# Kernel tuning notes

Measured on AMD Instinct MI355X. Metric: run time of the kernel, lower is better.

Reference implementation:

```python
import jax, jax.numpy as jnp
import numpy as np

EPS = 1e-6      # zero-token detection eps
LN_EPS = 1e-5   # torch LayerNorm default
H = 8           # num_heads


def setup_inputs() -> dict:
    key = jax.random.key(0)
    ks = jax.random.split(key, 6)
    B, T, D = 4, 2048, 512
    embs = jax.random.normal(ks[0], (B, T, D), jnp.float32)
    labels = jax.random.uniform(ks[1], (B, T), jnp.float32)
    s = 1.0 / np.sqrt(D)
    ln_g = jnp.ones((D,), jnp.float32)
    ln_b = jnp.zeros((D,), jnp.float32)
    in_proj_w = jax.random.uniform(ks[2], (3 * D, D), jnp.float32, -s, s)
    in_proj_b = jnp.zeros((3 * D,), jnp.float32)
    out_w = jax.random.uniform(ks[3], (D, D), jnp.float32, -s, s)
    out_b = jnp.zeros((D,), jnp.float32)
    alpha = jnp.float32(1.0)
    beta = jnp.float32(0.0)
    return {"embs": embs, "labels": labels, "ln_g": ln_g, "ln_b": ln_b,
            "in_proj_w": in_proj_w, "in_proj_b": in_proj_b,
            "out_w": out_w, "out_b": out_b, "alpha": alpha, "beta": beta}


def reference(embs, labels, ln_g, ln_b, in_proj_w, in_proj_b, out_w, out_b, alpha, beta):
    B, T, D = embs.shape
    h, dh = H, D // H
    # pre-LayerNorm
    mu = embs.mean(-1, keepdims=True)
    var = ((embs - mu) ** 2).mean(-1, keepdims=True)
    x = (embs - mu) / jnp.sqrt(var + LN_EPS) * ln_g + ln_b
    # key padding mask from all-zero tokens (computed on normalized x, as in source)
    kpm = jnp.abs(x).sum(-1) <= EPS                      # [B,T] bool
    w = jnp.where(kpm, jnp.float32(0.0), labels)         # zero labels on masked tokens
    # fused qkv projection (nn.MultiheadAttention in_proj)
    qkv = x @ in_proj_w.T + in_proj_b                    # [B,T,3D]
    q, k, v = jnp.split(qkv, 3, axis=-1)
    def sp(a):
        return a.reshape(B, T, h, dh).transpose(0, 2, 1, 3)  # [B,h,T,dh]
    q, k, v = sp(q), sp(k), sp(v)
    scores = jnp.einsum('bhqd,bhkd->bhqk', q, k) / np.sqrt(dh)
    # additive label bias: alpha * labels (broadcast over heads & queries) + beta
    scores = scores + (alpha * w[:, None, None, :] + beta)
    # key padding mask -> -inf (use large negative for stability)
    scores = jnp.where(kpm[:, None, None, :], jnp.float32(-1e30), scores)
    a = jax.nn.softmax(scores, axis=-1)
    o = jnp.einsum('bhqk,bhkd->bhqd', a, v).transpose(0, 2, 1, 3).reshape(B, T, D)
    o = o @ out_w.T + out_b
    o = jnp.nan_to_num(o, nan=0.0, posinf=0.0, neginf=0.0)
    # masked mean pool over T
    m = (~kpm)[..., None].astype(o.dtype)                # [B,T,1]
    pooled = (o * m).sum(1) / jnp.maximum(m.sum(1), 1.0)  # [B,D]
    return pooled
```

## Files before the change

kernel.cpp:

```cpp
#include <hip/hip_runtime.h>
#include <math.h>

#define T 2048
#define D 512
#define NH 8
#define DH 64
#define NB 4
#define NTOK (NB * T)
#define LOG2E 1.44269504f
#define QSCALE (0.125f * LOG2E)

using bf16x8 = __attribute__((ext_vector_type(8))) short;
using f32x4  = __attribute__((ext_vector_type(4))) float;

static __device__ __forceinline__ unsigned short f2bf(float f) {
    union { float f; unsigned u; } v; v.f = f;
    unsigned r = v.u + 0x7fffu + ((v.u >> 16) & 1u);
    return (unsigned short)(r >> 16);
}
#if __has_builtin(__builtin_amdgcn_cvt_pk_bf16_f32)
static __device__ __forceinline__ unsigned pack_bf16_pair(float a, float b) {
    auto r = __builtin_amdgcn_cvt_pk_bf16_f32(a, b);
    union { decltype(r) v; unsigned u; } c; c.v = r;
    return c.u;
}
#else
static __device__ __forceinline__ unsigned pack_bf16_pair(float a, float b) {
    union { float f; unsigned u; } ua, ub; ua.f = a; ub.f = b;
    unsigned ra = ua.u + 0x7fffu + ((ua.u >> 16) & 1u);
    unsigned rb = ub.u + 0x7fffu + ((ub.u >> 16) & 1u);
    return __builtin_amdgcn_perm(rb, ra, 0x07060302);
}
#endif


__global__ __launch_bounds__(256) void ln_kernel(
    const float* __restrict__ embs, const float* __restrict__ labels,
    const float* __restrict__ g, const float* __restrict__ bb,
    const float* __restrict__ alpha_p, const float* __restrict__ beta_p,
    unsigned short* __restrict__ xfrag, float* __restrict__ wexp,
    float* __restrict__ kpmf)
{
    __shared__ __align__(16) unsigned short Xs[16][520];
    int tid = threadIdx.x, wave = tid >> 6, lane = tid & 63;
    int quad = lane >> 4, lm = lane & 15;
    int t16 = blockIdx.x;

    float4 g0 = *(const float4*)(g + lane * 8), g1 = *(const float4*)(g + lane * 8 + 4);
    float4 c0 = *(const float4*)(bb + lane * 8), c1 = *(const float4*)(bb + lane * 8 + 4);
    float gv[8] = {g0.x, g0.y, g0.z, g0.w, g1.x, g1.y, g1.z, g1.w};
    float cv[8] = {c0.x, c0.y, c0.z, c0.w, c1.x, c1.y, c1.z, c1.w};

    for (int tt = 0; tt < 4; ++tt) {
        int n = t16 * 16 + wave * 4 + tt;
        const float* e = embs + (size_t)n * D + lane * 8;
        float4 a4 = *(const float4*)e, b4 = *(const float4*)(e + 4);
        float v[8] = {a4.x, a4.y, a4.z, a4.w, b4.x, b4.y, b4.z, b4.w};

        float s = 0.f, ss = 0.f;
        #pragma unroll
        for (int j = 0; j < 8; ++j) { s += v[j]; ss += v[j] * v[j]; }
        #pragma unroll
        for (int o = 1; o <= 32; o <<= 1) {
            s += __shfl_xor(s, o, 64);
            ss += __shfl_xor(ss, o, 64);
        }
        float mu = s * (1.0f / D);
        float var = ss * (1.0f / D) - mu * mu;
        float rstd = rsqrtf(var + 1e-5f);

        float x[8], as = 0.f;
        #pragma unroll
        for (int j = 0; j < 8; ++j) {
            x[j] = (v[j] - mu) * rstd * gv[j] + cv[j];
            as += fabsf(x[j]);
        }
        uint4 pk;
        pk.x = pack_bf16_pair(x[0], x[1]);
        pk.y = pack_bf16_pair(x[2], x[3]);
        pk.z = pack_bf16_pair(x[4], x[5]);
        pk.w = pack_bf16_pair(x[6], x[7]);
        *(uint4*)&Xs[wave * 4 + tt][lane * 8] = pk;

        #pragma unroll
        for (int o = 1; o <= 32; o <<= 1) as += __shfl_xor(as, o, 64);
        if (lane == 0) {
            int kpm = (as <= 1e-6f);
            kpmf[n] = kpm ? 1.0f : 0.0f;
            wexp[n] = kpm ? 0.0f : __expf(alpha_p[0] * labels[n] + beta_p[0]);
        }
    }
    __syncthreads();
    #pragma unroll
    for (int i = 0; i < 4; ++i) {
        int kc = wave * 4 + i;
        bf16x8 fr = *(const bf16x8*)&Xs[lm][kc * 32 + quad * 8];
        *(bf16x8*)(xfrag + ((size_t)(t16 * 16 + kc) * 64 + lane) * 8) = fr;
    }
}

__global__ __launch_bounds__(256) void wconv_kernel(
    const float* __restrict__ w, unsigned short* __restrict__ wbfrag)
{
    __shared__ __align__(16) unsigned short Ws[16][520];
    int tid = threadIdx.x, wave = tid >> 6, lane = tid & 63;
    int quad = lane >> 4, lm = lane & 15;
    int j16 = blockIdx.x;

    for (int tt = 0; tt < 4; ++tt) {
        int j = j16 * 16 + wave * 4 + tt;
        const float* wp = w + (size_t)j * D + lane * 8;
        float4 a4 = *(const float4*)wp, b4 = *(const float4*)(wp + 4);
        uint4 pk;
        pk.x = pack_bf16_pair(a4.x, a4.y);
        pk.y = pack_bf16_pair(a4.z, a4.w);
        pk.z = pack_bf16_pair(b4.x, b4.y);
        pk.w = pack_bf16_pair(b4.z, b4.w);
        *(uint4*)&Ws[wave * 4 + tt][lane * 8] = pk;
    }
    __syncthreads();
    #pragma unroll
    for (int i = 0; i < 4; ++i) {
        int kc = wave * 4 + i;
        bf16x8 fr = *(const bf16x8*)&Ws[lm][kc * 32 + quad * 8];
        *(bf16x8*)(wbfrag + ((size_t)(j16 * 16 + kc) * 64 + lane) * 8) = fr;
    }
}

__global__ __launch_bounds__(256) void wfrag_fill(
    const float* __restrict__ wexp, unsigned short* __restrict__ vfrag)
{
    int idx = blockIdx.x * 256 + threadIdx.x;
    int lane = idx & 63, chunk = idx >> 6;
    int kk = chunk & 1, t64 = (chunk >> 1) & 31, bh = chunk >> 6;
    int lm = lane & 15, quad = lane >> 4;
    int b_ = bh >> 3;
    size_t base = (((size_t)chunk * 5 + 4) * 64 + lane) * 8;
    if (lm == 0) {
        int key0 = t64 * 64 + kk * 32 + quad * 8;
        const float* wp = wexp + b_ * T + key0;
        unsigned short vv[8];
        #pragma unroll
        for (int e = 0; e < 8; ++e) vv[e] = f2bf(wp[e]);
        *(uint4*)(vfrag + base) = *(uint4*)vv;
    } else {
        uint4 z = {0u, 0u, 0u, 0u};
        *(uint4*)(vfrag + base) = z;
    }
}

__global__ __launch_bounds__(256) void qkv_mfma(
    const unsigned short* __restrict__ xfrag, const unsigned short* __restrict__ wbfrag,
    const float* __restrict__ bias, const float* __restrict__ wexp,
    unsigned short* __restrict__ qfrag, unsigned short* __restrict__ kfrag,
    unsigned short* __restrict__ vfrag)
{
    __shared__ __align__(16) unsigned short Ls[4][64][72];
    int tid = threadIdx.x;
    int wave = tid >> 6, lane = tid & 63, quad = lane >> 4, lm = lane & 15;
    int wr = wave >> 1, wc = wave & 1;
    int m0 = blockIdx.x * 128 + wr * 64;
    int j0 = blockIdx.y * 128 + wc * 64;
    int mt16 = m0 >> 4, jt16 = j0 >> 4;

    f32x4 acc[4][4];
    #pragma unroll
    for (int a = 0; a < 4; ++a)
        #pragma unroll
        for (int b = 0; b < 4; ++b) acc[a][b] = (f32x4){0.f,0.f,0.f,0.f};

    bf16x8 af0[4], bf0[4], af1[4], bf1[4];
    auto load_ab = [&](int kc, bf16x8 (&af)[4], bf16x8 (&bf)[4]) {
        #pragma unroll
        for (int mf = 0; mf < 4; ++mf)
            af[mf] = *(const bf16x8*)(xfrag + ((size_t)((mt16 + mf) * 16 + kc) * 64 + lane) * 8);
        #pragma unroll
        for (int nt = 0; nt < 4; ++nt)
            bf[nt] = *(const bf16x8*)(wbfrag + ((size_t)((jt16 + nt) * 16 + kc) * 64 + lane) * 8);
    };
    auto do_mfma = [&](bf16x8 (&af)[4], bf16x8 (&bf)[4]) {
        #pragma unroll
        for (int mf = 0; mf < 4; ++mf)
            #pragma unroll
            for (int nt = 0; nt < 4; ++nt)
                acc[mf][nt] = __builtin_amdgcn_mfma_f32_16x16x32_bf16(af[mf], bf[nt], acc[mf][nt], 0, 0, 0);
    };

    load_ab(0, af0, bf0);
    for (int kc = 0; kc < 16; kc += 2) {
        load_ab(kc + 1, af1, bf1);
        do_mfma(af0, bf0);
        load_ab((kc + 2) & 15, af0, bf0);
        do_mfma(af1, bf1);
    }

    int part = j0 >> 9;
    int h = (j0 & 511) >> 6;
    int b_ = m0 >> 11, tloc = m0 & (T - 1);
    int bh = b_ * NH + h;
    float bcol[4];
    #pragma unroll
    for (int nt = 0; nt < 4; ++nt) bcol[nt] = bias[j0 + nt * 16 + lm];

    if (part == 2) {
        float wv[4][4];
        #pragma unroll
        for (int mf = 0; mf < 4; ++mf)
            #pragma unroll
            for (int r = 0; r < 4; ++r)
                wv[mf][r] = wexp[b_ * T + tloc + mf * 16 + quad * 4 + r];
        #pragma unroll
        for (int mf = 0; mf < 4; ++mf)
            #pragma unroll
            for (int nt = 0; nt < 4; ++nt) {
                uint2 pw;
                pw.x = pack_bf16_pair((acc[mf][nt][0] + bcol[nt]) * wv[mf][0],
                                      (acc[mf][nt][1] + bcol[nt]) * wv[mf][1]);
                pw.y = pack_bf16_pair((acc[mf][nt][2] + bcol[nt]) * wv[mf][2],
                                      (acc[mf][nt][3] + bcol[nt]) * wv[mf][3]);
                *(uint2*)&Ls[wave][nt * 16 + lm][mf * 16 + quad * 4] = pw;
            }
        #pragma unroll
        for (int nt = 0; nt < 4; ++nt)
            #pragma unroll
            for (int kk = 0; kk < 2; ++kk) {
                bf16x8 fr = *(const bf16x8*)&Ls[wave][nt * 16 + lm][kk * 32 + quad * 8];
                size_t chunk = ((((size_t)bh * 32 + (tloc >> 6)) * 2 + kk) * 5) + nt;
                *(bf16x8*)(vfrag + chunk * 512 + lane * 8) = fr;
            }
    } else {
        float scale = (part == 0) ? QSCALE : 1.0f;
        #pragma unroll
        for (int mf = 0; mf < 4; ++mf)
            #pragma unroll
            for (int nt = 0; nt < 4; ++nt)
                #pragma unroll
                for (int r = 0; r < 4; ++r)
                    Ls[wave][mf * 16 + quad * 4 + r][nt * 16 + lm] =
                        f2bf((acc[mf][nt][r] + bcol[nt]) * scale);
        if (part == 0) {
            #pragma unroll
            for (int mf = 0; mf < 4; ++mf)
                #pragma unroll
                for (int kk = 0; kk < 2; ++kk) {
                    bf16x8 fr = *(const bf16x8*)&Ls[wave][mf * 16 + lm][kk * 32 + quad * 8];
                    size_t chunk = ((size_t)bh * 128 + (tloc >> 4) + mf) * 2 + kk;
                    *(bf16x8*)(qfrag + chunk * 512 + lane * 8) = fr;
                }
        } else {
            #pragma unroll
            for (int nta = 0; nta < 4; ++nta)
                #pragma unroll
                for (int kk = 0; kk < 2; ++kk) {
                    bf16x8 fr = *(const bf16x8*)&Ls[wave][lm * 4 + nta][kk * 32 + quad * 8];
                    size_t chunk = ((((size_t)bh * 32 + (tloc >> 6)) * 2 + kk) * 4) + nta;
                    *(bf16x8*)(kfrag + chunk * 512 + lane * 8) = fr;
                }
        }
    }
}

__global__ __launch_bounds__(256, 2) void attn_mfma(
    const unsigned short* __restrict__ qfrag, const unsigned short* __restrict__ kfrag,
    const unsigned short* __restrict__ vfrag, const float* __restrict__ kpmf,
    float* __restrict__ S)
{
    __shared__ __align__(16) unsigned short Ps[4][2][64][72];
    __shared__ float Lx[2][2][64];
    int g = blockIdx.x;
    int bh = g & 31, q0 = (g >> 5) * 128;
    int tid = threadIdx.x, wave = tid >> 6, lane = tid & 63;
    int quad = lane >> 4, lm = lane & 15;
    int qh = wave >> 1, ks = wave & 1;
    int qbase = q0 + qh * 64;
    int b_ = bh >> 3, h = bh & 7;

    bf16x8 qf[4][2];
    int t16b = (qbase >> 4);
    #pragma unroll
    for (int mf = 0; mf < 4; ++mf)
        #pragma unroll
        for (int kk = 0; kk < 2; ++kk)
            qf[mf][kk] = *(const bf16x8*)(qfrag +
                (((size_t)(bh * 128 + t16b + mf) * 2 + kk) * 64 + lane) * 8);

    f32x4 accO[4][4], accL[4];
    #pragma unroll
    for (int mf = 0; mf < 4; ++mf) {
        #pragma unroll
        for (int nt = 0; nt < 4; ++nt) accO[mf][nt] = (f32x4){0.f,0.f,0.f,0.f};
        accL[mf] = (f32x4){0.f,0.f,0.f,0.f};
    }

    const unsigned short* kb = kfrag + (size_t)bh * 32 * 8 * 512 + (size_t)lane * 8;
    const unsigned short* vb = vfrag + (size_t)bh * 32 * 10 * 512 + (size_t)lane * 8;
    int t0k = ks * 16;

    bf16x8 kf[4][2];
    auto load_k = [&](int t64) {
        const unsigned short* p = kb + (size_t)t64 * 8 * 512;
        #pragma unroll
        for (int kk = 0; kk < 2; ++kk)
            #pragma unroll
            for (int nt = 0; nt < 4; ++nt)
                kf[nt][kk] = *(const bf16x8*)(p + ((size_t)kk * 4 + nt) * 512);
    };
    auto load_v = [&](int t64, bf16x8 (&vf)[5][2]) {
        const unsigned short* p = vb + (size_t)t64 * 10 * 512;
        #pragma unroll
        for (int kk = 0; kk < 2; ++kk)
            #pragma unroll
            for (int nt = 0; nt < 5; ++nt)
                vf[nt][kk] = *(const bf16x8*)(p + ((size_t)kk * 5 + nt) * 512);
    };
    auto load_p = [&](int buf, bf16x8 (&pf)[4][2]) {
        #pragma unroll
        for (int mf = 0; mf < 4; ++mf)
            #pragma unroll
            for (int kk = 0; kk < 2; ++kk)
                pf[mf][kk] = *(const bf16x8*)&Ps[wave][buf][mf * 16 + lm][kk * 32 + quad * 8];
    };
    auto qk_exp = [&](int buf) {
        #pragma unroll
        for (int mf = 0; mf < 4; ++mf) {
            f32x4 s[4];
            __builtin_amdgcn_s_setprio(1);
            #pragma unroll
            for (int nt = 0; nt < 4; ++nt) {
                f32x4 t0 = (f32x4){0.f,0.f,0.f,0.f};
                t0 = __builtin_amdgcn_mfma_f32_16x16x32_bf16(qf[mf][0], kf[nt][0], t0, 0, 0, 0);
                t0 = __builtin_amdgcn_mfma_f32_16x16x32_bf16(qf[mf][1], kf[nt][1], t0, 0, 0, 0);
                s[nt] = t0;
            }
            __builtin_amdgcn_s_setprio(0);
            int rowb = mf * 16 + quad * 4;
            #pragma unroll
            for (int r = 0; r < 4; ++r) {
                float p0 = __builtin_amdgcn_exp2f(s[0][r]);
                float p1 = __builtin_amdgcn_exp2f(s[1][r]);
                float p2 = __builtin_amdgcn_exp2f(s[2][r]);
                float p3 = __builtin_amdgcn_exp2f(s[3][r]);
                uint2 pw;
                pw.x = pack_bf16_pair(p0, p1);
                pw.y = pack_bf16_pair(p2, p3);
                *(uint2*)&Ps[wave][buf][rowb + r][lm * 4] = pw;
            }
        }
    };
    auto pv = [&](bf16x8 (&pf)[4][2], bf16x8 (&vf)[5][2]) {
        __builtin_amdgcn_s_setprio(1);
        #pragma unroll
        for (int mf = 0; mf < 4; ++mf) {
            #pragma unroll
            for (int nt = 0; nt < 4; ++nt) {
                accO[mf][nt] = __builtin_amdgcn_mfma_f32_16x16x32_bf16(pf[mf][0], vf[nt][0], accO[mf][nt], 0, 0, 0);
                accO[mf][nt] = __builtin_amdgcn_mfma_f32_16x16x32_bf16(pf[mf][1], vf[nt][1], accO[mf][nt], 0, 0, 0);
            }
            accL[mf] = __builtin_amdgcn_mfma_f32_16x16x32_bf16(pf[mf][0], vf[4][0], accL[mf], 0, 0, 0);
            accL[mf] = __builtin_amdgcn_mfma_f32_16x16x32_bf16(pf[mf][1], vf[4][1], accL[mf], 0, 0, 0);
        }
        __builtin_amdgcn_s_setprio(0);
    };

    load_k(t0k);
    qk_exp(0);
    load_k(t0k + 1);
    for (int t = 1; t < 16; ++t) {
        bf16x8 pf[4][2], vf[5][2];
        load_p((t - 1) & 1, pf);
        load_v(t0k + t - 1, vf);
        qk_exp(t & 1);
        load_k(t0k + ((t + 1) & 15));
        pv(pf, vf);
    }
    {
        bf16x8 pf[4][2], vf[5][2];
        load_p(1, pf);
        load_v(t0k + 15, vf);
        pv(pf, vf);
    }

    if (lm == 0) {
        #pragma unroll
        for (int mf = 0; mf < 4; ++mf)
            #pragma unroll
            for (int r = 0; r < 4; ++r)
                Lx[qh][ks][mf * 16 + quad * 4 + r] = accL[mf][r];
    }
    __syncthreads();

    float pooled[4] = {0.f, 0.f, 0.f, 0.f};
    #pragma unroll
    for (int mf = 0; mf < 4; ++mf)
        #pragma unroll
        for (int r = 0; r < 4; ++r) {
            int rloc = mf * 16 + quad * 4 + r;
            float l = Lx[qh][0][rloc] + Lx[qh][1][rloc];
            float w = (1.0f - kpmf[b_ * T + qbase + rloc]) / l;
            #pragma unroll
            for (int nt = 0; nt < 4; ++nt) pooled[nt] += accO[mf][nt][r] * w;
        }
    #pragma unroll
    for (int nt = 0; nt < 4; ++nt) {
        pooled[nt] += __shfl_xor(pooled[nt], 16, 64);
        pooled[nt] += __shfl_xor(pooled[nt], 32, 64);
    }
    if (quad == 0) {
        #pragma unroll
        for (int nt = 0; nt < 4; ++nt)
            atomicAdd(&S[b_ * D + h * DH + nt * 16 + lm], pooled[nt]);
    }
}

__global__ __launch_bounds__(256) void out_kernel(
    const float* __restrict__ S, const float* __restrict__ kpmf,
    const float* __restrict__ Wo, const float* __restrict__ bo,
    float* __restrict__ out)
{
    __shared__ float Sl[512];
    __shared__ float cs[4];
    __shared__ float pr[4][64];
    int b_ = blockIdx.x >> 3;
    int cg = blockIdx.x & 7;
    int tid = threadIdx.x;
    int col = tid & 63, kq = tid >> 6;
    Sl[tid] = S[b_ * D + tid];
    Sl[tid + 256] = S[b_ * D + tid + 256];
    const float* kp = kpmf + b_ * T;
    float c = 0.f;
    for (int t = tid; t < T; t += 256) c += kp[t];
    #pragma unroll
    for (int o = 32; o; o >>= 1) c += __shfl_xor(c, o, 64);
    if ((tid & 63) == 0) cs[tid >> 6] = c;
    __syncthreads();
    float masked = cs[0] + cs[1] + cs[2] + cs[3];
    float cnt = (float)T - masked;
    float inv = 1.0f / fmaxf(cnt, 1.0f);

    int d = cg * 64 + col;
    const float4* wr4 = (const float4*)(Wo + (size_t)d * D + kq * 128);
    float dot = 0.f;
    #pragma unroll 8
    for (int i = 0; i < 32; ++i) {
        float4 w4 = wr4[i];
        int kbase = kq * 128 + i * 4;
        dot += Sl[kbase + 0] * w4.x + Sl[kbase + 1] * w4.y +
               Sl[kbase + 2] * w4.z + Sl[kbase + 3] * w4.w;
    }
    pr[kq][col] = dot;
    __syncthreads();
    if (kq == 0) {
        float tot = pr[0][col] + pr[1][col] + pr[2][col] + pr[3][col];
        out[b_ * D + d] = (tot + bo[d] * cnt) * inv;
    }
}

extern "C" void kernel_launch(void* const* d_in, const int* in_sizes, int n_in,
                              void* d_out, int out_size, void* d_ws, size_t ws_size,
                              hipStream_t stream) {
    const float* embs   = (const float*)d_in[0];
    const float* labels = (const float*)d_in[1];
    const float* ln_g   = (const float*)d_in[2];
    const float* ln_b   = (const float*)d_in[3];
    const float* ipw    = (const float*)d_in[4];
    const float* ipb    = (const float*)d_in[5];
    const float* ow     = (const float*)d_in[6];
    const float* obb    = (const float*)d_in[7];
    const float* alpha  = (const float*)d_in[8];
    const float* beta   = (const float*)d_in[9];
    float* out = (float*)d_out;

    unsigned short* xfrag  = (unsigned short*)d_ws;
    unsigned short* wbfrag = xfrag + (size_t)NTOK * D;
    unsigned short* qfrag  = wbfrag + (size_t)3 * D * D;
    unsigned short* kfrag  = qfrag + (size_t)NTOK * D;
    unsigned short* vfrag  = kfrag + (size_t)NTOK * D;
    float* wexp = (float*)(vfrag + (size_t)32 * 32 * 2 * 5 * 512);
    float* kpmf = wexp + NTOK;
    float* S    = kpmf + NTOK;

    hipMemsetAsync(S, 0, (size_t)NB * D * sizeof(float), stream);
    ln_kernel<<<NTOK / 16, 256, 0, stream>>>(embs, labels, ln_g, ln_b, alpha, beta,
                                             xfrag, wexp, kpmf);
    wconv_kernel<<<(3 * D) / 16, 256, 0, stream>>>(ipw, wbfrag);
    wfrag_fill<<<512, 256, 0, stream>>>(wexp, vfrag);
    dim3 gq(NTOK / 128, (3 * D) / 128);
    qkv_mfma<<<gq, 256, 0, stream>>>(xfrag, wbfrag, ipb, wexp, qfrag, kfrag, vfrag);
    attn_mfma<<<32 * (T / 128), 256, 0, stream>>>(qfrag, kfrag, vfrag, kpmf, S);
    out_kernel<<<NB * 8, 256, 0, stream>>>(S, kpmf, ow, obb, out);
}
```

Measured before the change: 157.2 us.

## Merge LayerNorm, weight conversion and memset into one prep kernel; fold wexp fill into QKV

Combines the LayerNorm, in-projection weight bf16 conversion and the S-accumulator zeroing into one kernel, using block-index ranges to assign each role. The separate wexp fragment fill kernel is removed, and its work moves into the V epilogue of the QKV GEMM. This cuts the pipeline from six launches (including a memset) to three before attention, removing launch and inter-kernel gap overhead. The cost is some extra divergence and global reads in the QKV epilogue.

Result: faster. 150.6 us, median of 2 (-4.2%).

```diff
diff --git a/kernel.cpp b/kernel.cpp
--- a/kernel.cpp
+++ b/kernel.cpp
@@ -34,118 +34,100 @@
 #endif
 
 
-__global__ __launch_bounds__(256) void ln_kernel(
+__global__ __launch_bounds__(256) void prep_kernel(
     const float* __restrict__ embs, const float* __restrict__ labels,
     const float* __restrict__ g, const float* __restrict__ bb,
     const float* __restrict__ alpha_p, const float* __restrict__ beta_p,
+    const float* __restrict__ ipw,
     unsigned short* __restrict__ xfrag, float* __restrict__ wexp,
-    float* __restrict__ kpmf)
+    float* __restrict__ kpmf, unsigned short* __restrict__ wbfrag,
+    float* __restrict__ S)
 {
-    __shared__ __align__(16) unsigned short Xs[16][520];
+    __shared__ __align__(16) unsigned short Sh[16][520];
+    int blk = blockIdx.x;
     int tid = threadIdx.x, wave = tid >> 6, lane = tid & 63;
     int quad = lane >> 4, lm = lane & 15;
-    int t16 = blockIdx.x;
-
-    float4 g0 = *(const float4*)(g + lane * 8), g1 = *(const float4*)(g + lane * 8 + 4);
-    float4 c0 = *(const float4*)(bb + lane * 8), c1 = *(const float4*)(bb + lane * 8 + 4);
-    float gv[8] = {g0.x, g0.y, g0.z, g0.w, g1.x, g1.y, g1.z, g1.w};
-    float cv[8] = {c0.x, c0.y, c0.z, c0.w, c1.x, c1.y, c1.z, c1.w};
-
-    for (int tt = 0; tt < 4; ++tt) {
-        int n = t16 * 16 + wave * 4 + tt;
-        const float* e = embs + (size_t)n * D + lane * 8;
-        float4 a4 = *(const float4*)e, b4 = *(const float4*)(e + 4);
-        float v[8] = {a4.x, a4.y, a4.z, a4.w, b4.x, b4.y, b4.z, b4.w};
-
-        float s = 0.f, ss = 0.f;
-        #pragma unroll
-        for (int j = 0; j < 8; ++j) { s += v[j]; ss += v[j] * v[j]; }
-        #pragma unroll
-        for (int o = 1; o <= 32; o <<= 1) {
-            s += __shfl_xor(s, o, 64);
-            ss += __shfl_xor(ss, o, 64);
-        }
-        float mu = s * (1.0f / D);
-        float var = ss * (1.0f / D) - mu * mu;
-        float rstd = rsqrtf(var + 1e-5f);
-
-        float x[8], as = 0.f;
-        #pragma unroll
-        for (int j = 0; j < 8; ++j) {
-            x[j] = (v[j] - mu) * rstd * gv[j] + cv[j];
-            as += fabsf(x[j]);
-        }
-        uint4 pk;
-        pk.x = pack_bf16_pair(x[0], x[1]);
-        pk.y = pack_bf16_pair(x[2], x[3]);
-        pk.z = pack_bf16_pair(x[4], x[5]);
-        pk.w = pack_bf16_pair(x[6], x[7]);
-        *(uint4*)&Xs[wave * 4 + tt][lane * 8] = pk;
-
-        #pragma unroll
-        for (int o = 1; o <= 32; o <<= 1) as += __shfl_xor(as, o, 64);
-        if (lane == 0) {
-            int kpm = (as <= 1e-6f);
-            kpmf[n] = kpm ? 1.0f : 0.0f;
-            wexp[n] = kpm ? 0.0f : __expf(alpha_p[0] * labels[n] + beta_p[0]);
-        }
-    }
-    __syncthreads();
-    #pragma unroll
-    for (int i = 0; i < 4; ++i) {
-        int kc = wave * 4 + i;
-        bf16x8 fr = *(const bf16x8*)&Xs[lm][kc * 32 + quad * 8];
-        *(bf16x8*)(xfrag + ((size_t)(t16 * 16 + kc) * 64 + lane) * 8) = fr;
-    }
-}
-
-__global__ __launch_bounds__(256) void wconv_kernel(
-    const float* __restrict__ w, unsigned short* __restrict__ wbfrag)
-{
-    __shared__ __align__(16) unsigned short Ws[16][520];
-    int tid = threadIdx.x, wave = tid >> 6, lane = tid & 63;
-    int quad = lane >> 4, lm = lane & 15;
-    int j16 = blockIdx.x;
-
-    for (int tt = 0; tt < 4; ++tt) {
-        int j = j16 * 16 + wave * 4 + tt;
-        const float* wp = w + (size_t)j * D + lane * 8;
-        float4 a4 = *(const float4*)wp, b4 = *(const float4*)(wp + 4);
-        uint4 pk;
-        pk.x = pack_bf16_pair(a4.x, a4.y);
-        pk.y = pack_bf16_pair(a4.z, a4.w);
-        pk.z = pack_bf16_pair(b4.x, b4.y);
-        pk.w = pack_bf16_pair(b4.z, b4.w);
-        *(uint4*)&Ws[wave * 4 + tt][lane * 8] = pk;
-    }
-    __syncthreads();
-    #pragma unroll
-    for (int i = 0; i < 4; ++i) {
-        int kc = wave * 4 + i;
-        bf16x8 fr = *(const bf16x8*)&Ws[lm][kc * 32 + quad * 8];
-        *(bf16x8*)(wbfrag + ((size_t)(j16 * 16 + kc) * 64 + lane) * 8) = fr;
-    }
-}
-
-__global__ __launch_bounds__(256) void wfrag_fill(
-    const float* __restrict__ wexp, unsigned short* __restrict__ vfrag)
-{
-    int idx = blockIdx.x * 256 + threadIdx.x;
-    int lane = idx & 63, chunk = idx >> 6;
-    int kk = chunk & 1, t64 = (chunk >> 1) & 31, bh = chunk >> 6;
-    int lm = lane & 15, quad = lane >> 4;
-    int b_ = bh >> 3;
-    size_t base = (((size_t)chunk * 5 + 4) * 64 + lane) * 8;
-    if (lm == 0) {
-        int key0 = t64 * 64 + kk * 32 + quad * 8;
-        const float* wp = wexp + b_ * T + key0;
-        unsigned short vv[8];
-        #pragma unroll
-        for (int e = 0; e < 8; ++e) vv[e] = f2bf(wp[e]);
-        *(uint4*)(vfrag + base) = *(uint4*)vv;
+
+    if (blk >= 608) {
+        float4 z = {0.f, 0.f, 0.f, 0.f};
+        ((float4*)S)[tid] = z;
+        ((float4*)S)[tid + 256] = z;
+        return;
+    }
+
+    if (blk < 512) {
+        int t16 = blk;
+        float4 g0 = *(const float4*)(g + lane * 8), g1 = *(const float4*)(g + lane * 8 + 4);
+        float4 c0 = *(const float4*)(bb + lane * 8), c1 = *(const float4*)(bb + lane * 8 + 4);
+        float gv[8] = {g0.x, g0.y, g0.z, g0.w, g1.x, g1.y, g1.z, g1.w};
+        float cv[8] = {c0.x, c0.y, c0.z, c0.w, c1.x, c1.y, c1.z, c1.w};
+
+        for (int tt = 0; tt < 4; ++tt) {
+            int n = t16 * 16 + wave * 4 + tt;
+            const float* e = embs + (size_t)n * D + lane * 8;
+            float4 a4 = *(const float4*)e, b4 = *(const float4*)(e + 4);
+            float v[8] = {a4.x, a4.y, a4.z, a4.w, b4.x, b4.y, b4.z, b4.w};
+
+            float s = 0.f, ss = 0.f;
+            #pragma unroll
+            for (int j = 0; j < 8; ++j) { s += v[j]; ss += v[j] * v[j]; }
+            #pragma unroll
+            for (int o = 1; o <= 32; o <<= 1) {
+                s += __shfl_xor(s, o, 64);
+                ss += __shfl_xor(ss, o, 64);
+            }
+            float mu = s * (1.0f / D);
+            float var = ss * (1.0f / D) - mu * mu;
+            float rstd = rsqrtf(var + 1e-5f);
+
+            float x[8], as = 0.f;
+            #pragma unroll
+            for (int j = 0; j < 8; ++j) {
+                x[j] = (v[j] - mu) * rstd * gv[j] + cv[j];
+                as += fabsf(x[j]);
+            }
+            uint4 pk;
+            pk.x = pack_bf16_pair(x[0], x[1]);
+            pk.y = pack_bf16_pair(x[2], x[3]);
+            pk.z = pack_bf16_pair(x[4], x[5]);
+            pk.w = pack_bf16_pair(x[6], x[7]);
+            *(uint4*)&Sh[wave * 4 + tt][lane * 8] = pk;
+
+            #pragma unroll
+            for (int o = 1; o <= 32; o <<= 1) as += __shfl_xor(as, o, 64);
+            if (lane == 0) {
+                int kpm = (as <= 1e-6f);
+                kpmf[n] = kpm ? 1.0f : 0.0f;
+                wexp[n] = kpm ? 0.0f : __expf(alpha_p[0] * labels[n] + beta_p[0]);
+            }
+        }
+        __syncthreads();
+        #pragma unroll
+        for (int i = 0; i < 4; ++i) {
+            int kc = wave * 4 + i;
+            bf16x8 fr = *(const bf16x8*)&Sh[lm][kc * 32 + quad * 8];
+            *(bf16x8*)(xfrag + ((size_t)(t16 * 16 + kc) * 64 + lane) * 8) = fr;
+        }
     } else {
-        uint4 z = {0u, 0u, 0u, 0u};
-        *(uint4*)(vfrag + base) = z;
+        int j16 = blk - 512;
+        for (int tt = 0; tt < 4; ++tt) {
+            int j = j16 * 16 + wave * 4 + tt;
+            const float* wp = ipw + (size_t)j * D + lane * 8;
+            float4 a4 = *(const float4*)wp, b4 = *(const float4*)(wp + 4);
+            uint4 pk;
+            pk.x = pack_bf16_pair(a4.x, a4.y);
+            pk.y = pack_bf16_pair(a4.z, a4.w);
+            pk.z = pack_bf16_pair(b4.x, b4.y);
+            pk.w = pack_bf16_pair(b4.z, b4.w);
+            *(uint4*)&Sh[wave * 4 + tt][lane * 8] = pk;
+        }
+        __syncthreads();
+        #pragma unroll
+        for (int i = 0; i < 4; ++i) {
+            int kc = wave * 4 + i;
+            bf16x8 fr = *(const bf16x8*)&Sh[lm][kc * 32 + quad * 8];
+            *(bf16x8*)(wbfrag + ((size_t)(j16 * 16 + kc) * 64 + lane) * 8) = fr;
+        }
     }
 }
 
@@ -228,6 +210,19 @@
                 size_t chunk = ((((size_t)bh * 32 + (tloc >> 6)) * 2 + kk) * 5) + nt;
                 *(bf16x8*)(vfrag + chunk * 512 + lane * 8) = fr;
             }
+        #pragma unroll
+        for (int kk = 0; kk < 2; ++kk) {
+            size_t chunk = ((((size_t)bh * 32 + (tloc >> 6)) * 2 + kk) * 5) + 4;
+            uint4 pk = {0u, 0u, 0u, 0u};
+            if (lm == 0) {
+                const float* wp = wexp + b_ * T + tloc + kk * 32 + quad * 8;
+                unsigned short vv[8];
+                #pragma unroll
+                for (int e = 0; e < 8; ++e) vv[e] = f2bf(wp[e]);
+                pk = *(uint4*)vv;
+            }
+            *(uint4*)(vfrag + chunk * 512 + (size_t)lane * 8) = pk;
+        }
     } else {
         float scale = (part == 0) ? QSCALE : 1.0f;
         #pragma unroll
@@ -479,11 +474,8 @@
     float* kpmf = wexp + NTOK;
     float* S    = kpmf + NTOK;
 
-    hipMemsetAsync(S, 0, (size_t)NB * D * sizeof(float), stream);
-    ln_kernel<<<NTOK / 16, 256, 0, stream>>>(embs, labels, ln_g, ln_b, alpha, beta,
-                                             xfrag, wexp, kpmf);
-    wconv_kernel<<<(3 * D) / 16, 256, 0, stream>>>(ipw, wbfrag);
-    wfrag_fill<<<512, 256, 0, stream>>>(wexp, vfrag);
+    prep_kernel<<<609, 256, 0, stream>>>(embs, labels, ln_g, ln_b, alpha, beta,
+                                         ipw, xfrag, wexp, kpmf, wbfrag, S);
     dim3 gq(NTOK / 128, (3 * D) / 128);
     qkv_mfma<<<gq, 256, 0, stream>>>(xfrag, wbfrag, ipb, wexp, qfrag, kfrag, vfrag);
     attn_mfma<<<32 * (T / 128), 256, 0, stream>>>(qfrag, kfrag, vfrag, kpmf, S);
```
